# Kernel optimization log

Hardware: AMD Instinct MI355X
Metric: run time of the kernel (lower is better)

The kernel has to match this reference:

```python
import jax, jax.numpy as jnp
import numpy as np

N = 1_000_000   # number of input points
C = 32          # feature channels
S = 64          # spatial size per dim (and batch-key range)

def _linear_keys(coords):
    # coords: [N, 4] int32 -> unique int64 key per (x, y, z, batch)
    c = coords.astype(jnp.int64)
    return ((c[:, 0] * S + c[:, 1]) * S + c[:, 2]) * S + c[:, 3]

def setup_inputs() -> dict:
    key = jax.random.key(0)
    k1, k2 = jax.random.split(key)
    coords = jax.random.randint(k1, (N, 4), 0, S, dtype=jnp.int32)
    features = jax.random.normal(k2, (N, C), dtype=jnp.float32)
    return {"coords": coords, "features": features}

def reference(coords, features):
    # SCN InputLayer, mode=3 (sum duplicates): dedupe coordinate keys,
    # scatter-add features of duplicate points into the unique voxel row.
    keys = _linear_keys(coords)                       # [N] int64
    # fixed-size unique for jit compatibility; padding rows get no contributions
    _, inv = jnp.unique(keys, size=N, fill_value=-1, return_inverse=True)
    out = jax.ops.segment_sum(features, inv, num_segments=N)  # [N, C]
    return out
```

## Files before the change

### kernel.cpp

```cpp
#include <hip/hip_runtime.h>


constexpr int S = 64;
constexpr int KEYSPACE = S * S * S * S;
constexpr int NWORDS   = KEYSPACE / 32;
constexpr int SCAN_BLK = 256;
constexpr int NSCANBLK = NWORDS / SCAN_BLK;

__global__ void k_setbits(const int4* __restrict__ coords,
                          unsigned* __restrict__ bitmap,
                          unsigned* __restrict__ keys, int n) {
    int i = blockIdx.x * blockDim.x + threadIdx.x;
    if (i >= n) return;
    int4 c = coords[i];
    unsigned key = (unsigned)(((c.x * S + c.y) * S + c.z) * S + c.w);
    unsigned bit = 1u << (key & 31);
    unsigned old = atomicOr(&bitmap[key >> 5], bit);
    keys[i] = key | ((old & bit) ? 0u : 0x80000000u);
}

__global__ void k_blocksums(const unsigned* __restrict__ bitmap,
                            unsigned* __restrict__ blockSums) {
    int w = blockIdx.x * SCAN_BLK + threadIdx.x;
    unsigned pc = __popc(bitmap[w]);
    for (int off = 32; off > 0; off >>= 1) pc += __shfl_down(pc, off);
    __shared__ unsigned sm[SCAN_BLK / 64];
    if ((threadIdx.x & 63) == 0) sm[threadIdx.x >> 6] = pc;
    __syncthreads();
    if (threadIdx.x == 0) {
        unsigned s = 0;
        for (int j = 0; j < SCAN_BLK / 64; ++j) s += sm[j];
        blockSums[blockIdx.x] = s;
    }
}

__global__ void k_scan(const unsigned* __restrict__ blockSums,
                       unsigned* __restrict__ blockOffs,
                       unsigned* __restrict__ d_total) {
    __shared__ unsigned tsum[256];
    int t = threadIdx.x;
    unsigned v[8];
    unsigned s = 0;
    for (int j = 0; j < 8; ++j) { v[j] = blockSums[t * 8 + j]; s += v[j]; }
    tsum[t] = s;
    __syncthreads();
    unsigned pre = 0;
    for (int j = 0; j < t; ++j) pre += tsum[j];
    for (int j = 0; j < 8; ++j) { blockOffs[t * 8 + j] = pre; pre += v[j]; }
    if (t == 255) d_total[0] = pre;
}

__global__ void k_meta(const unsigned* __restrict__ bitmap,
                       const unsigned* __restrict__ blockOffs,
                       uint2* __restrict__ meta) {
    int t = threadIdx.x;
    int w = blockIdx.x * SCAN_BLK + t;
    unsigned bits = bitmap[w];
    unsigned pc = __popc(bits);
    unsigned inc = pc;
    for (int off = 1; off < 64; off <<= 1) {
        unsigned x = __shfl_up(inc, off);
        if ((t & 63) >= off) inc += x;
    }
    __shared__ unsigned wsum[SCAN_BLK / 64];
    if ((t & 63) == 63) wsum[t >> 6] = inc;
    __syncthreads();
    unsigned base = 0;
    for (int j = 0; j < (t >> 6); ++j) base += wsum[j];
    meta[w] = make_uint2(bits, blockOffs[blockIdx.x] + base + (inc - pc));
}

__global__ void k_scatter1(const unsigned* __restrict__ keys,
                           const float4* __restrict__ feats4,
                           const uint2* __restrict__ meta,
                           float4* __restrict__ out4, int n) {
    int gid = blockIdx.x * blockDim.x + threadIdx.x;
    int i = gid >> 3;
    if (i >= n) return;
    unsigned kw = keys[i];
    if (!(kw & 0x80000000u)) return;
    unsigned key = kw & 0x00FFFFFFu;
    uint2 m = meta[key >> 5];
    unsigned rank = m.y + __popc(m.x & ((1u << (key & 31)) - 1u));
    int c4 = gid & 7;
    out4[(long long)rank * 8 + c4] = feats4[(long long)i * 8 + c4];
}

__global__ void k_scatter2(const unsigned* __restrict__ keys,
                           const float* __restrict__ feats,
                           const uint2* __restrict__ meta,
                           float* __restrict__ out, int n) {
    int i = blockIdx.x * blockDim.x + threadIdx.x;
    if (i >= n) return;
    unsigned kw = keys[i];
    if (kw & 0x80000000u) return;
    unsigned key = kw & 0x00FFFFFFu;
    uint2 m = meta[key >> 5];
    unsigned rank = m.y + __popc(m.x & ((1u << (key & 31)) - 1u));
    const float* f = feats + (long long)i * 32;
    float* o = out + (long long)rank * 32;
#pragma unroll
    for (int c = 0; c < 32; ++c) atomicAdd(&o[c], f[c]);
}

__global__ void k_tailzero(float4* __restrict__ out4,
                           const unsigned* __restrict__ d_total, int n) {
    unsigned nU = *d_total;
    long long start = (long long)nU * 8;
    long long end   = (long long)n * 8;
    long long stride = (long long)gridDim.x * blockDim.x;
    for (long long idx = start + blockIdx.x * (long long)blockDim.x + threadIdx.x;
         idx < end; idx += stride)
        out4[idx] = make_float4(0.f, 0.f, 0.f, 0.f);
}

extern "C" void kernel_launch(void* const* d_in, const int* in_sizes, int n_in,
                              void* d_out, int out_size, void* d_ws, size_t ws_size,
                              hipStream_t stream) {
    const int4*   coords = (const int4*)d_in[0];
    const float*  feats  = (const float*)d_in[1];
    const float4* feats4 = (const float4*)d_in[1];
    float*  out  = (float*)d_out;
    float4* out4 = (float4*)d_out;
    int n = in_sizes[0] / 4;
    if (n <= 0) return;

    unsigned* bitmap    = (unsigned*)d_ws;
    uint2*    meta      = (uint2*)(bitmap + NWORDS);
    unsigned* keys      = bitmap + NWORDS + 2 * NWORDS;
    unsigned* blockSums = keys + n;
    unsigned* blockOffs = blockSums + NSCANBLK;
    unsigned* d_total   = blockOffs + NSCANBLK;

    hipMemsetAsync(bitmap, 0, (size_t)NWORDS * sizeof(unsigned), stream);

    k_setbits<<<(n + 255) / 256, 256, 0, stream>>>(coords, bitmap, keys, n);
    k_blocksums<<<NSCANBLK, SCAN_BLK, 0, stream>>>(bitmap, blockSums);
    k_scan<<<1, 256, 0, stream>>>(blockSums, blockOffs, d_total);
    k_meta<<<NSCANBLK, SCAN_BLK, 0, stream>>>(bitmap, blockOffs, meta);

    long long lanes = (long long)n * 8;
    k_scatter1<<<(int)((lanes + 255) / 256), 256, 0, stream>>>(keys, feats4, meta, out4, n);
    k_scatter2<<<(n + 255) / 256, 256, 0, stream>>>(keys, feats, meta, out, n);
    k_tailzero<<<512, 256, 0, stream>>>(out4, d_total, n);
}
```

Measured before the change: 341.0 us.

## Compact duplicate points into a list and fuse atomic scatter with tail zeroing

During bit setting, each wave ballot-compacts the indices of duplicate (losing) points into a list using one atomic counter increment per wave. A single grid-stride kernel then walks only that list for the atomic feature sums and also zeroes the output tail, replacing two launches. This avoids a full pass over all N points for the second scatter. The change also adds nontemporal loads and stores and a wave-shuffle prefix sum in the scan kernel, which replaces the quadratic per-thread serial sum. It adds an extra counter atomic and list writes in the first kernel.

```diff
diff --git a/kernel.cpp b/kernel.cpp
--- a/kernel.cpp
+++ b/kernel.cpp
@@ -7,16 +7,36 @@
 constexpr int SCAN_BLK = 256;
 constexpr int NSCANBLK = NWORDS / SCAN_BLK;
 
-__global__ void k_setbits(const int4* __restrict__ coords,
+typedef float f4 __attribute__((ext_vector_type(4)));
+typedef int   i4 __attribute__((ext_vector_type(4)));
+
+__global__ void k_setbits(const i4* __restrict__ coords,
                           unsigned* __restrict__ bitmap,
-                          unsigned* __restrict__ keys, int n) {
+                          unsigned* __restrict__ keys,
+                          unsigned* __restrict__ loserList,
+                          unsigned* __restrict__ ctr, int n) {
     int i = blockIdx.x * blockDim.x + threadIdx.x;
-    if (i >= n) return;
-    int4 c = coords[i];
-    unsigned key = (unsigned)(((c.x * S + c.y) * S + c.z) * S + c.w);
-    unsigned bit = 1u << (key & 31);
-    unsigned old = atomicOr(&bitmap[key >> 5], bit);
-    keys[i] = key | ((old & bit) ? 0u : 0x80000000u);
+    bool valid = i < n;
+    bool loser = false;
+    if (valid) {
+        i4 c = __builtin_nontemporal_load(&coords[i]);
+        unsigned key = (unsigned)(((c[0] * S + c[1]) * S + c[2]) * S + c[3]);
+        unsigned bit = 1u << (key & 31);
+        unsigned old = atomicOr(&bitmap[key >> 5], bit);
+        bool win = !(old & bit);
+        loser = !win;
+        keys[i] = key | (win ? 0x80000000u : 0u);
+    }
+    unsigned lane = threadIdx.x & 63u;
+    unsigned long long mask = __ballot(loser);
+    unsigned count = (unsigned)__popcll(mask);
+    unsigned base = 0;
+    if (lane == 0 && count) base = atomicAdd(ctr, count);
+    base = __shfl(base, 0);
+    if (loser) {
+        unsigned pre = (unsigned)__popcll(mask & ((1ull << lane) - 1ull));
+        loserList[base + pre] = (unsigned)i;
+    }
 }
 
 __global__ void k_blocksums(const unsigned* __restrict__ bitmap,
@@ -37,17 +57,25 @@
 __global__ void k_scan(const unsigned* __restrict__ blockSums,
                        unsigned* __restrict__ blockOffs,
                        unsigned* __restrict__ d_total) {
-    __shared__ unsigned tsum[256];
     int t = threadIdx.x;
+    unsigned lane = t & 63u;
+    int wave = t >> 6;
     unsigned v[8];
     unsigned s = 0;
     for (int j = 0; j < 8; ++j) { v[j] = blockSums[t * 8 + j]; s += v[j]; }
-    tsum[t] = s;
+    unsigned inc = s;
+    for (int off = 1; off < 64; off <<= 1) {
+        unsigned x = __shfl_up(inc, off);
+        if (lane >= off) inc += x;
+    }
+    __shared__ unsigned wtot[4];
+    if (lane == 63) wtot[wave] = inc;
     __syncthreads();
-    unsigned pre = 0;
-    for (int j = 0; j < t; ++j) pre += tsum[j];
-    for (int j = 0; j < 8; ++j) { blockOffs[t * 8 + j] = pre; pre += v[j]; }
-    if (t == 255) d_total[0] = pre;
+    unsigned wbase = 0;
+    for (int j = 0; j < wave; ++j) wbase += wtot[j];
+    unsigned excl = wbase + inc - s;
+    for (int j = 0; j < 8; ++j) { blockOffs[t * 8 + j] = excl; excl += v[j]; }
+    if (t == 0) d_total[0] = wtot[0] + wtot[1] + wtot[2] + wtot[3];
 }
 
 __global__ void k_meta(const unsigned* __restrict__ bitmap,
@@ -71,9 +99,9 @@
 }
 
 __global__ void k_scatter1(const unsigned* __restrict__ keys,
-                           const float4* __restrict__ feats4,
+                           const f4* __restrict__ feats4,
                            const uint2* __restrict__ meta,
-                           float4* __restrict__ out4, int n) {
+                           f4* __restrict__ out4, int n) {
     int gid = blockIdx.x * blockDim.x + threadIdx.x;
     int i = gid >> 3;
     if (i >= n) return;
@@ -83,64 +111,70 @@
     uint2 m = meta[key >> 5];
     unsigned rank = m.y + __popc(m.x & ((1u << (key & 31)) - 1u));
     int c4 = gid & 7;
-    out4[(long long)rank * 8 + c4] = feats4[(long long)i * 8 + c4];
+    f4 f = __builtin_nontemporal_load(&feats4[(long long)i * 8 + c4]);
+    __builtin_nontemporal_store(f, &out4[(long long)rank * 8 + c4]);
 }
 
-__global__ void k_scatter2(const unsigned* __restrict__ keys,
-                           const float* __restrict__ feats,
-                           const uint2* __restrict__ meta,
-                           float* __restrict__ out, int n) {
-    int i = blockIdx.x * blockDim.x + threadIdx.x;
-    if (i >= n) return;
-    unsigned kw = keys[i];
-    if (kw & 0x80000000u) return;
-    unsigned key = kw & 0x00FFFFFFu;
-    uint2 m = meta[key >> 5];
-    unsigned rank = m.y + __popc(m.x & ((1u << (key & 31)) - 1u));
-    const float* f = feats + (long long)i * 32;
-    float* o = out + (long long)rank * 32;
+__global__ void k_losers_tail(const unsigned* __restrict__ keys,
+                              const float* __restrict__ feats,
+                              const uint2* __restrict__ meta,
+                              const unsigned* __restrict__ loserList,
+                              const unsigned* __restrict__ ctr,
+                              const unsigned* __restrict__ d_total,
+                              float* __restrict__ out,
+                              f4* __restrict__ out4, int n) {
+    unsigned nLosers = ctr[0];
+    int tid = blockIdx.x * blockDim.x + threadIdx.x;
+    int stride = gridDim.x * blockDim.x;
+    for (unsigned i = tid; i < nLosers; i += stride) {
+        unsigned idx = loserList[i];
+        unsigned key = keys[idx] & 0x00FFFFFFu;
+        uint2 m = meta[key >> 5];
+        unsigned rank = m.y + __popc(m.x & ((1u << (key & 31)) - 1u));
+        const float* f = feats + (long long)idx * 32;
+        float* o = out + (long long)rank * 32;
 #pragma unroll
-    for (int c = 0; c < 32; ++c) atomicAdd(&o[c], f[c]);
-}
-
-__global__ void k_tailzero(float4* __restrict__ out4,
-                           const unsigned* __restrict__ d_total, int n) {
-    unsigned nU = *d_total;
+        for (int c = 0; c < 32; ++c) atomicAdd(&o[c], f[c]);
+    }
+    unsigned nU = d_total[0];
     long long start = (long long)nU * 8;
     long long end   = (long long)n * 8;
-    long long stride = (long long)gridDim.x * blockDim.x;
-    for (long long idx = start + blockIdx.x * (long long)blockDim.x + threadIdx.x;
-         idx < end; idx += stride)
-        out4[idx] = make_float4(0.f, 0.f, 0.f, 0.f);
+    for (long long idx = start + tid; idx < end; idx += stride) {
+        f4 z = {0.f, 0.f, 0.f, 0.f};
+        __builtin_nontemporal_store(z, &out4[idx]);
+    }
 }
 
 extern "C" void kernel_launch(void* const* d_in, const int* in_sizes, int n_in,
                               void* d_out, int out_size, void* d_ws, size_t ws_size,
                               hipStream_t stream) {
-    const int4*   coords = (const int4*)d_in[0];
-    const float*  feats  = (const float*)d_in[1];
-    const float4* feats4 = (const float4*)d_in[1];
-    float*  out  = (float*)d_out;
-    float4* out4 = (float4*)d_out;
+    const i4*    coords = (const i4*)d_in[0];
+    const float* feats  = (const float*)d_in[1];
+    const f4*    feats4 = (const f4*)d_in[1];
+    float* out  = (float*)d_out;
+    f4*    out4 = (f4*)d_out;
     int n = in_sizes[0] / 4;
     if (n <= 0) return;
 
-    unsigned* bitmap    = (unsigned*)d_ws;
+    unsigned* ctr       = (unsigned*)d_ws;
+    unsigned* bitmap    = ctr + 2;
     uint2*    meta      = (uint2*)(bitmap + NWORDS);
     unsigned* keys      = bitmap + NWORDS + 2 * NWORDS;
-    unsigned* blockSums = keys + n;
+    unsigned* loserList = keys + n;
+    unsigned* blockSums = loserList + n;
     unsigned* blockOffs = blockSums + NSCANBLK;
     unsigned* d_total   = blockOffs + NSCANBLK;
 
-    hipMemsetAsync(bitmap, 0, (size_t)NWORDS * sizeof(unsigned), stream);
+    hipMemsetAsync(d_ws, 0, (size_t)(2 + NWORDS) * sizeof(unsigned), stream);
 
-    k_setbits<<<(n + 255) / 256, 256, 0, stream>>>(coords, bitmap, keys, n);
+    k_setbits<<<(n + 255) / 256, 256, 0, stream>>>(coords, bitmap, keys,
+                                                   loserList, ctr, n);
     k_blocksums<<<NSCANBLK, SCAN_BLK, 0, stream>>>(bitmap, blockSums);
     k_scan<<<1, 256, 0, stream>>>(blockSums, blockOffs, d_total);
     k_meta<<<NSCANBLK, SCAN_BLK, 0, stream>>>(bitmap, blockOffs, meta);
 
     long long lanes = (long long)n * 8;
     k_scatter1<<<(int)((lanes + 255) / 256), 256, 0, stream>>>(keys, feats4, meta, out4, n);
-    k_scatter2<<<(n + 255) / 256, 256, 0, stream>>>(keys, feats, meta, out, n);
-    k_tailzero<<<512, 256, 0, stream>>>(out4, d_total, n);
+    k_losers_tail<<<256, 256, 0, stream>>>(keys, feats, meta, loserList, ctr,
+                                           d_total, out, out4, n);
 }
```

Result: slower. 450.0 us (+32.0%).
